# Kernel tuning notes

Hardware: AMD Instinct MI355X
Metric: run time of the kernel (lower is better)

The kernel has to match this reference:

```python
import jax, jax.numpy as jnp
import numpy as np
from jax import lax


def _haar_filters():
    c = np.float32(1.0 / np.sqrt(2.0))
    lo = np.array([c, c], np.float32)   # db1 dec_lo reversed == rec_lo == [c, c]
    hi = np.array([c, -c], np.float32)  # db1 dec_hi reversed == rec_hi == [c, -c]
    # filters[k][i, j] built exactly as in the torch source (outer products)
    dec = np.stack([np.outer(lo, lo) / 2.0, np.outer(hi, lo), np.outer(lo, hi), np.outer(hi, hi)]).astype(np.float32)
    inv = np.stack([np.outer(lo, lo) * 2.0, np.outer(hi, lo), np.outer(lo, hi), np.outer(hi, hi)]).astype(np.float32)
    return jnp.asarray(dec), jnp.asarray(inv)

DEC, INV = _haar_filters()  # each [4, 2, 2]


def wt(x):
    # depthwise Haar DWT, stride-2 2x2 conv per channel, then (v+1)/2 on high bands
    B, C, H, W = x.shape
    xr = x.reshape(B, C, H // 2, 2, W // 2, 2)
    out = jnp.einsum('bchiwj,kij->bckhw', xr, DEC)  # [B, C, 4, H/2, W/2]
    out = jnp.concatenate([out[:, :, :1], (out[:, :, 1:] + 1.0) * 0.5], axis=2)
    return out.reshape(B, 4 * C, H // 2, W // 2)


def iwt(v):
    # undo affine (2v-1 on high bands), then depthwise 2x2-stride-2 transpose conv
    B, C4, H, W = v.shape
    C = C4 // 4
    vr = v.reshape(B, C, 4, H, W)
    vr = jnp.concatenate([vr[:, :, :1], 2.0 * vr[:, :, 1:] - 1.0], axis=2)
    out = jnp.einsum('bckhw,kij->bchiwj', vr, INV)  # place each pixel into a 2x2 block
    return out.reshape(B, C, 2 * H, 2 * W)


def conv3x3(x, w, b):
    y = lax.conv_general_dilated(x, w, (1, 1), ((1, 1), (1, 1)),
                                 dimension_numbers=('NCHW', 'OIHW', 'NCHW'))
    return y + b[None, :, None, None]


def lrelu(x):
    return jnp.where(x >= 0, x, 0.2 * x)


def setup_inputs() -> dict:
    key = jax.random.key(0)
    ks = jax.random.split(key, 32)
    c = 16
    s = 0.02
    def w(k, shp):
        return jax.random.normal(ks[k], shp, jnp.float32) * s
    inp = {
        'x': jax.random.normal(ks[0], (4, 3, 256, 256), jnp.float32),
        'conv1_w': w(1, (c, 12, 3, 3)),        'conv1_b': w(2, (c,)),
        'conv2_w': w(3, (4 * c, 4 * c, 3, 3)), 'conv2_b': w(4, (4 * c,)),
        'conv3_w': w(5, (16 * c, 16 * c, 3, 3)), 'conv3_b': w(6, (16 * c,)),
        'conv4_w': w(7, (64 * c, 64 * c, 3, 3)), 'conv4_b': w(8, (64 * c,)),
        'convd4_w': w(9, (16 * c, 32 * c, 3, 3)), 'convd4_b': w(10, (16 * c,)),
        'convd3_w': w(11, (4 * c, 8 * c, 3, 3)), 'convd3_b': w(12, (4 * c,)),
        'convd2_w': w(13, (c, 2 * c, 3, 3)),    'convd2_b': w(14, (c,)),
        'convd1_w': w(15, (12, c, 3, 3)),       'convd1_b': w(16, (12,)),
        'cfin_w': w(17, (3, 3, 1, 1)),
    }
    return inp


def reference(x, conv1_w, conv1_b, conv2_w, conv2_b, conv3_w, conv3_b,
              conv4_w, conv4_b, convd4_w, convd4_b, convd3_w, convd3_b,
              convd2_w, convd2_b, convd1_w, convd1_b, cfin_w):
    w1 = wt(x)
    c1 = lrelu(conv3x3(w1, conv1_w, conv1_b))
    w2 = wt(c1)
    c2 = lrelu(conv3x3(w2, conv2_w, conv2_b))
    w3 = wt(c2)
    c3 = lrelu(conv3x3(w3, conv3_w, conv3_b))
    w4 = wt(c3)
    c4 = lrelu(conv3x3(w4, conv4_w, conv4_b))
    c5 = lrelu(conv3x3(c4, conv4_w, conv4_b))
    c6 = conv3x3(c5, conv4_w, conv4_b)
    ic4 = lrelu(c6 + w4)
    iw4 = jnp.concatenate([c3, iwt(ic4)], axis=1)
    ic3 = lrelu(conv3x3(iw4, convd4_w, convd4_b))
    iw3 = jnp.concatenate([c2, iwt(ic3)], axis=1)
    ic2 = lrelu(conv3x3(iw3, convd3_w, convd3_b))
    iw2 = jnp.concatenate([c1, iwt(ic2)], axis=1)
    ic1 = lrelu(conv3x3(iw2, convd2_w, convd2_b))
    iw1 = lrelu(conv3x3(ic1, convd1_w, convd1_b))
    y = iwt(iw1)
    # final 1x1 conv, no bias
    return jnp.einsum('bchw,oc->bohw', y, cfin_w[:, :, 0, 0])
```

## Files before the change

### kernel.cpp

```cpp
#include <hip/hip_runtime.h>


#define TPB 256

typedef _Float16 f16x8 __attribute__((ext_vector_type(8)));
typedef float f32x4 __attribute__((ext_vector_type(4)));

#define GLOAD_LDS16(g, l)                                                     \
    __builtin_amdgcn_global_load_lds(                                         \
        (const __attribute__((address_space(1))) void*)(g),                   \
        (__attribute__((address_space(3))) void*)(l), 16, 0, 0)

__global__ __launch_bounds__(TPB) void wt_k(const float* __restrict__ src,
                                            float* __restrict__ dst,
                                            int C, int H2, int W2) {
    int n = C * H2 * W2;
    int idx = blockIdx.x * TPB + threadIdx.x;
    if (idx >= n) return;
    int b = blockIdx.z;
    int c = idx / (H2 * W2);
    int p = idx - c * (H2 * W2);
    int h = p / W2, w = p - h * W2;
    int W = 2 * W2;
    const float* r = src + (((size_t)b * C + c) * (2 * H2) + 2 * h) * W + 2 * w;
    float a = r[0], bb = r[1], cc = r[W], dd = r[W + 1];
    size_t st = (size_t)H2 * W2;
    float* o = dst + (((size_t)b * 4 * C + 4 * c) * st) + p;
    o[0]      = 0.25f * (a + bb + cc + dd);
    o[st]     = (0.5f * (a + bb - cc - dd) + 1.0f) * 0.5f;
    o[2 * st] = (0.5f * (a - bb + cc - dd) + 1.0f) * 0.5f;
    o[3 * st] = (0.5f * (a - bb - cc + dd) + 1.0f) * 0.5f;
}

template <int LC>
__global__ __launch_bounds__(TPB) void wt_cl_k(const float* __restrict__ src,
                                               _Float16* __restrict__ X,
                                               int H2, int W2) {
    const int C = 1 << LC;
    int idx = blockIdx.x * TPB + threadIdx.x;
    int b = blockIdx.z;
    int c = idx & (C - 1);
    int p = idx >> LC;
    if (p >= H2 * W2) return;
    int h = p / W2, w = p - h * W2;
    int W = 2 * W2;
    const float* r = src + (((size_t)b * C + c) * (2 * H2) + 2 * h) * W + 2 * w;
    float a = r[0], bb = r[1], cc = r[W], dd = r[W + 1];
    _Float16* o = X + ((size_t)(b * H2 * W2 + p)) * (4 * C) + 4 * c;
    o[0] = (_Float16)(0.25f * (a + bb + cc + dd));
    o[1] = (_Float16)((0.5f * (a + bb - cc - dd) + 1.0f) * 0.5f);
    o[2] = (_Float16)((0.5f * (a - bb + cc - dd) + 1.0f) * 0.5f);
    o[3] = (_Float16)((0.5f * (a - bb - cc + dd) + 1.0f) * 0.5f);
}

__global__ __launch_bounds__(TPB) void iwt_k(const float* __restrict__ src,
                                             float* __restrict__ dst,
                                             int C, int H, int W) {
    int n = C * H * W;
    int idx = blockIdx.x * TPB + threadIdx.x;
    if (idx >= n) return;
    int b = blockIdx.z;
    int c = idx / (H * W);
    int p = idx - c * (H * W);
    int h = p / W, w = p - h * W;
    size_t st = (size_t)H * W;
    const float* r = src + ((size_t)b * 4 * C + 4 * c) * st + p;
    float v0 = r[0];
    float v1 = 2.0f * r[st] - 1.0f;
    float v2 = 2.0f * r[2 * st] - 1.0f;
    float v3 = 2.0f * r[3 * st] - 1.0f;
    float* o = dst + (((size_t)b * C + c) * (2 * H) + 2 * h) * (2 * W) + 2 * w;
    o[0]         = v0 + 0.5f * ( v1 + v2 + v3);
    o[1]         = v0 + 0.5f * ( v1 - v2 - v3);
    o[2 * W]     = v0 + 0.5f * (-v1 + v2 - v3);
    o[2 * W + 1] = v0 + 0.5f * (-v1 - v2 + v3);
}

template <int LC>
__global__ __launch_bounds__(TPB) void iwt_cl_k(const float* __restrict__ src,
                                                _Float16* __restrict__ X,
                                                int H, int W, int Coff, int Ctot) {
    const int C = 1 << LC;
    int idx = blockIdx.x * TPB + threadIdx.x;
    int b = blockIdx.z;
    int c = idx & (C - 1);
    int p = idx >> LC;
    if (p >= H * W) return;
    int h = p / W, w = p - h * W;
    size_t st = (size_t)H * W;
    const float* r = src + ((size_t)b * 4 * C + 4 * c) * st + p;
    float v0 = r[0];
    float v1 = 2.0f * r[st] - 1.0f;
    float v2 = 2.0f * r[2 * st] - 1.0f;
    float v3 = 2.0f * r[3 * st] - 1.0f;
    size_t mb = (size_t)b * 4 * H * W + (size_t)(2 * h) * (2 * W) + 2 * w;
    _Float16* o = X + mb * Ctot + Coff + c;
    o[0]                          = (_Float16)(v0 + 0.5f * ( v1 + v2 + v3));
    o[(size_t)Ctot]               = (_Float16)(v0 + 0.5f * ( v1 - v2 - v3));
    o[(size_t)(2 * W) * Ctot]     = (_Float16)(v0 + 0.5f * (-v1 + v2 - v3));
    o[(size_t)(2 * W + 1) * Ctot] = (_Float16)(v0 + 0.5f * (-v1 - v2 + v3));
}

template <int CO, bool LRELU, bool HAS_SKIP>
__global__ __launch_bounds__(TPB) void conv3x3_k(
    const float* __restrict__ s0, int C0,
    const float* __restrict__ s1,
    const float* __restrict__ wgt, const float* __restrict__ bias,
    const float* __restrict__ skip,
    float* __restrict__ out,
    int Cin, int Cout, int H, int W) {
    const int hw = H * W;
    int p = blockIdx.x * TPB + threadIdx.x;
    if (p >= hw) return;
    const int b = blockIdx.z;
    const int cog = blockIdx.y * CO;
    const int h = p / W, w = p - (p / W) * W;
    const bool hm = h > 0, hp = h < H - 1, wm = w > 0, wpp = w < W - 1;

    float acc[CO];
#pragma unroll
    for (int i = 0; i < CO; i++) acc[i] = bias[cog + i];

    const int C1n = Cin - C0;
    for (int ci = 0; ci < Cin; ci++) {
        const float* sp = (ci < C0)
            ? s0 + ((size_t)b * C0 + ci) * hw
            : s1 + ((size_t)b * C1n + (ci - C0)) * hw;
        const float* r = sp + p;
        float x00 = (hm && wm)  ? r[-W - 1] : 0.0f;
        float x01 = hm          ? r[-W]     : 0.0f;
        float x02 = (hm && wpp) ? r[-W + 1] : 0.0f;
        float x10 = wm          ? r[-1]     : 0.0f;
        float x11 =               r[0];
        float x12 = wpp         ? r[1]      : 0.0f;
        float x20 = (hp && wm)  ? r[W - 1]  : 0.0f;
        float x21 = hp          ? r[W]      : 0.0f;
        float x22 = (hp && wpp) ? r[W + 1]  : 0.0f;
        const float* wk = wgt + ((size_t)cog * Cin + ci) * 9;
#pragma unroll
        for (int i = 0; i < CO; i++) {
            const float* wi = wk + (size_t)i * Cin * 9;
            acc[i] += x00 * wi[0] + x01 * wi[1] + x02 * wi[2]
                    + x10 * wi[3] + x11 * wi[4] + x12 * wi[5]
                    + x20 * wi[6] + x21 * wi[7] + x22 * wi[8];
        }
    }
#pragma unroll
    for (int i = 0; i < CO; i++) {
        float v = acc[i];
        if (HAS_SKIP) v += skip[((size_t)b * Cout + cog + i) * hw + p];
        if (LRELU) v = (v >= 0.0f) ? v : 0.2f * v;
        out[((size_t)b * Cout + cog + i) * hw + p] = v;
    }
}


__global__ __launch_bounds__(TPB) void wtrans_g_k(const float* __restrict__ w,
                                                  _Float16* __restrict__ Bh,
                                                  int Cin, int n) {
    int idx = blockIdx.x * TPB + threadIdx.x;
    if (idx >= n) return;
    int K = 9 * Cin;
    int co = idx / K;
    int r = idx - co * K;
    int tap = r / Cin, ci = r - tap * Cin;
    Bh[idx] = (_Float16)w[((size_t)co * Cin + ci) * 9 + tap];
}

__global__ __launch_bounds__(TPB) void bias_mc_k(float* __restrict__ C,
                                                 const float* __restrict__ bias,
                                                 int mask) {
    int idx = blockIdx.x * TPB + threadIdx.x;
    C[idx] = bias[idx & mask];
}

__global__ __launch_bounds__(TPB) void w4_to_x_k(const float* __restrict__ W4,
                                                 _Float16* __restrict__ X) {
    int idx = blockIdx.x * TPB + threadIdx.x;
    int m = idx >> 10, ci = idx & 1023;
    int b = m >> 8, p = m & 255;
    X[idx] = (_Float16)W4[(((size_t)b << 10) + ci) * 256 + p];
}

template <int LC, int NT>
__global__ __launch_bounds__(TPB) void cgemm_k(
    const _Float16* __restrict__ X,
    const _Float16* __restrict__ Bw,
    float* __restrict__ Cout,
    int Wimg, int kc, int N) {
    constexpr int CIN = 1 << LC;
    constexpr int K = 9 << LC;
    const int HW = Wimg * Wimg;
    const int m0 = blockIdx.x * 128;
    const int n0 = blockIdx.y * (NT * 32);
    const int k0 = blockIdx.z * kc;
    const int iters = kc >> 5;

    __shared__ _Float16 As[128 * 32];
    __shared__ _Float16 Bs[NT * 32 * 32];

    const int tid = threadIdx.x;
    const int wave = tid >> 6, lane = tid & 63;
    const int wm = (wave >> 1) * 64;
    const int wn = (wave & 1) * (NT * 16);

    const int r0 = tid >> 2;
    const int colh = (tid & 3) * 8;
    int rbase[2], rh[2], rw[2];
#pragma unroll
    for (int q = 0; q < 2; q++) {
        int m = m0 + r0 + q * 64;
        int b = m / HW;
        int p = m - b * HW;
        rh[q] = p / Wimg;
        rw[q] = p - rh[q] * Wimg;
        rbase[q] = b * HW;
    }
    _Float16* lA0 = &As[r0 * 32 + colh];
    _Float16* lA1 = &As[(r0 + 64) * 32 + colh];

    const int f = tid * 16;
    const int brow = f >> 6, bbyte = f & 63;
    const char* gB[NT / 2];
#pragma unroll
    for (int q = 0; q < NT / 2; q++)
        gB[q] = (const char*)Bw + ((size_t)(n0 + brow + q * 64) * K + k0) * 2 + bbyte;

    f32x4 acc[4][NT];
#pragma unroll
    for (int i = 0; i < 4; i++)
#pragma unroll
        for (int j = 0; j < NT; j++) acc[i][j] = {0.f, 0.f, 0.f, 0.f};

    const int frow = lane & 15;
    const int fkh = (lane >> 4) * 8;

    for (int it = 0; it < iters; ++it) {
        const int kk = k0 + (it << 5);
        const int tap = kk >> LC;
        const int ci0 = kk & (CIN - 1);
        const int t3 = tap / 3;
        const int dh = t3 - 1;
        const int dw = tap - t3 * 3 - 1;
#pragma unroll
        for (int q = 0; q < 2; q++) {
            int hh = rh[q] + dh, ww = rw[q] + dw;
            f16x8 v = {0, 0, 0, 0, 0, 0, 0, 0};
            if ((unsigned)hh < (unsigned)Wimg && (unsigned)ww < (unsigned)Wimg)
                v = *(const f16x8*)(X + (((size_t)(rbase[q] + hh * Wimg + ww)) << LC)
                                      + ci0 + colh);
            if (q == 0) *(f16x8*)lA0 = v;
            else        *(f16x8*)lA1 = v;
        }
#pragma unroll
        for (int q = 0; q < NT / 2; q++) {
            GLOAD_LDS16(gB[q], (char*)Bs + f + q * 4096);
            gB[q] += 64;
        }
        __syncthreads();

        f16x8 af[4], bf[NT];
#pragma unroll
        for (int mt = 0; mt < 4; mt++)
            af[mt] = *(const f16x8*)&As[(wm + mt * 16 + frow) * 32 + fkh];
#pragma unroll
        for (int nt = 0; nt < NT; nt++)
            bf[nt] = *(const f16x8*)&Bs[(wn + nt * 16 + frow) * 32 + fkh];
#pragma unroll
        for (int mt = 0; mt < 4; mt++)
#pragma unroll
            for (int nt = 0; nt < NT; nt++)
                acc[mt][nt] = __builtin_amdgcn_mfma_f32_16x16x32_f16(
                    af[mt], bf[nt], acc[mt][nt], 0, 0, 0);
        __syncthreads();
    }

    const int cm = m0 + wm + (lane >> 4) * 4;
    const int cn = n0 + wn + (lane & 15);
#pragma unroll
    for (int mt = 0; mt < 4; mt++)
#pragma unroll
        for (int nt = 0; nt < NT; nt++)
#pragma unroll
            for (int r = 0; r < 4; r++)
                unsafeAtomicAdd(&Cout[(size_t)(cm + mt * 16 + r) * N + cn + nt * 16],
                                acc[mt][nt][r]);
}

template <bool SPAT, bool CL>
__global__ __launch_bounds__(TPB) void fin_cl_k(const float* __restrict__ Cm,
                                                float* __restrict__ spat,
                                                _Float16* __restrict__ X,
                                                int LN, int LHW, int Coff, int Ctot) {
    int idx = blockIdx.x * TPB + threadIdx.x;
    int m = idx >> LN;
    int c = idx & ((1 << LN) - 1);
    float v = Cm[idx];
    v = (v >= 0.0f) ? v : 0.2f * v;
    if (SPAT) {
        int b = m >> LHW;
        int p = m & ((1 << LHW) - 1);
        spat[(((size_t)(b << LN) + c) << LHW) + p] = v;
    }
    if (CL) X[(size_t)m * Ctot + Coff + c] = (_Float16)v;
}

__global__ __launch_bounds__(TPB) void fin_sp_k(const float* __restrict__ C,
                                                const float* __restrict__ W4,
                                                float* __restrict__ out) {
    int idx = blockIdx.x * TPB + threadIdx.x;
    int b = idx >> 18;
    int r = idx & 262143;
    int c = r >> 8, p = r & 255;
    int m = (b << 8) + p;
    float v = C[(size_t)m * 1024 + c] + W4[idx];
    out[idx] = (v >= 0.0f) ? v : 0.2f * v;
}

__global__ __launch_bounds__(TPB) void final_k(const float* __restrict__ src,
                                               const float* __restrict__ cf,
                                               float* __restrict__ out) {
    int p = blockIdx.x * TPB + threadIdx.x;
    int b = blockIdx.z;
    int h = p >> 7, w = p & 127;
    const int st = 128 * 128;
    float y00[3], y01[3], y10[3], y11[3];
    const float* r = src + (size_t)b * 12 * st + p;
#pragma unroll
    for (int c = 0; c < 3; c++) {
        float v0 = r[(4 * c) * st];
        float v1 = 2.0f * r[(4 * c + 1) * st] - 1.0f;
        float v2 = 2.0f * r[(4 * c + 2) * st] - 1.0f;
        float v3 = 2.0f * r[(4 * c + 3) * st] - 1.0f;
        y00[c] = v0 + 0.5f * ( v1 + v2 + v3);
        y01[c] = v0 + 0.5f * ( v1 - v2 - v3);
        y10[c] = v0 + 0.5f * (-v1 + v2 - v3);
        y11[c] = v0 + 0.5f * (-v1 - v2 + v3);
    }
#pragma unroll
    for (int o = 0; o < 3; o++) {
        float k0 = cf[o * 3], k1 = cf[o * 3 + 1], k2 = cf[o * 3 + 2];
        float* q = out + (((size_t)b * 3 + o) * 256 + 2 * h) * 256 + 2 * w;
        q[0]   = k0 * y00[0] + k1 * y00[1] + k2 * y00[2];
        q[1]   = k0 * y01[0] + k1 * y01[1] + k2 * y01[2];
        q[256] = k0 * y10[0] + k1 * y10[1] + k2 * y10[2];
        q[257] = k0 * y11[0] + k1 * y11[1] + k2 * y11[2];
    }
}

static inline void conv_launch(const float* s0, int C0, const float* s1,
                               const float* wgt, const float* bias,
                               float* out, int Cin, int Cout, int H, int W,
                               int CO, hipStream_t st) {
    dim3 grid((H * W + TPB - 1) / TPB, Cout / CO, 4);
    if (CO == 8)
        conv3x3_k<8, true, false><<<grid, TPB, 0, st>>>(s0, C0, s1, wgt, bias, nullptr, out, Cin, Cout, H, W);
    else
        conv3x3_k<4, true, false><<<grid, TPB, 0, st>>>(s0, C0, s1, wgt, bias, nullptr, out, Cin, Cout, H, W);
}

extern "C" void kernel_launch(void* const* d_in, const int* in_sizes, int n_in,
                              void* d_out, int out_size, void* d_ws, size_t ws_size,
                              hipStream_t stream) {
    (void)in_sizes; (void)n_in; (void)out_size; (void)ws_size;
    const float* x      = (const float*)d_in[0];
    const float* c1w    = (const float*)d_in[1];
    const float* c1b    = (const float*)d_in[2];
    const float* c2w    = (const float*)d_in[3];
    const float* c2b    = (const float*)d_in[4];
    const float* c3w    = (const float*)d_in[5];
    const float* c3b    = (const float*)d_in[6];
    const float* c4w    = (const float*)d_in[7];
    const float* c4b    = (const float*)d_in[8];
    const float* d4w    = (const float*)d_in[9];
    const float* d4b    = (const float*)d_in[10];
    const float* d3w    = (const float*)d_in[11];
    const float* d3b    = (const float*)d_in[12];
    const float* d2w    = (const float*)d_in[13];
    const float* d2b    = (const float*)d_in[14];
    const float* d1w    = (const float*)d_in[15];
    const float* d1b    = (const float*)d_in[16];
    const float* cfin   = (const float*)d_in[17];
    float* out = (float*)d_out;

    char* base = (char*)d_ws;
    const size_t MB = 1 << 20;
    float*    C1   = (float*)(base + 0 * MB);
    float*    C3   = (float*)(base + 4 * MB);
    float*    W4   = (float*)(base + 8 * MB);
    float*    TA   = (float*)(base + 12 * MB);
    float*    TB   = (float*)(base + 16 * MB);
    float*    C2   = (float*)(base + 20 * MB);
    float*    Cmc  = (float*)(base + 24 * MB);
    _Float16* X0   = (_Float16*)(base + 28 * MB);
    _Float16* X1   = (_Float16*)(base + 30 * MB);
    _Float16* Xa   = (_Float16*)(base + 32 * MB);
    _Float16* Xd3  = (_Float16*)(base + 34 * MB);
    _Float16* Xd4  = (_Float16*)(base + 38 * MB);
    _Float16* Bh4  = (_Float16*)(base + 42 * MB);
    _Float16* Bh3  = (_Float16*)(base + 60 * MB);
    _Float16* Bhd4 = (_Float16*)(base + 62 * MB);
    _Float16* Bhd3 = (_Float16*)(base + 65 * MB);
    _Float16* Bh2  = (_Float16*)(base + 66 * MB);

    wtrans_g_k<<<36864, TPB, 0, stream>>>(c4w, Bh4, 1024, 9437184);
    wtrans_g_k<<<2304,  TPB, 0, stream>>>(c3w, Bh3, 256, 589824);
    wtrans_g_k<<<4608,  TPB, 0, stream>>>(d4w, Bhd4, 512, 1179648);
    wtrans_g_k<<<288,   TPB, 0, stream>>>(d3w, Bhd3, 128, 73728);
    wtrans_g_k<<<144,   TPB, 0, stream>>>(c2w, Bh2, 64, 36864);

    wt_k<<<dim3(192, 1, 4), TPB, 0, stream>>>(x, TA, 3, 128, 128);
    conv_launch(TA, 12, nullptr, c1w, c1b, C1, 12, 16, 128, 128, 8, stream);
    wt_cl_k<4><<<dim3(256, 1, 4), TPB, 0, stream>>>(C1, Xa, 64, 64);
    bias_mc_k<<<4096, TPB, 0, stream>>>(Cmc, c2b, 63);
    cgemm_k<6, 2><<<dim3(128, 1, 2), TPB, 0, stream>>>(Xa, Bh2, Cmc, 64, 288, 64);
    fin_cl_k<true, true><<<4096, TPB, 0, stream>>>(Cmc, C2, Xd3, 6, 12, 0, 128);
    wt_cl_k<6><<<dim3(256, 1, 4), TPB, 0, stream>>>(C2, Xa, 32, 32);
    bias_mc_k<<<4096, TPB, 0, stream>>>(Cmc, c3b, 255);
    cgemm_k<8, 4><<<dim3(32, 2, 4), TPB, 0, stream>>>(Xa, Bh3, Cmc, 32, 576, 256);
    fin_cl_k<true, true><<<4096, TPB, 0, stream>>>(Cmc, C3, Xd4, 8, 10, 0, 512);
    wt_k<<<dim3(256, 1, 4), TPB, 0, stream>>>(C3, W4, 256, 16, 16);
    w4_to_x_k<<<4096, TPB, 0, stream>>>(W4, X0);
    bias_mc_k<<<4096, TPB, 0, stream>>>(Cmc, c4b, 1023);
    cgemm_k<10, 4><<<dim3(8, 8, 8), TPB, 0, stream>>>(X0, Bh4, Cmc, 16, 1152, 1024);
    fin_cl_k<false, true><<<4096, TPB, 0, stream>>>(Cmc, nullptr, X1, 10, 8, 0, 1024);
    bias_mc_k<<<4096, TPB, 0, stream>>>(Cmc, c4b, 1023);
    cgemm_k<10, 4><<<dim3(8, 8, 8), TPB, 0, stream>>>(X1, Bh4, Cmc, 16, 1152, 1024);
    fin_cl_k<false, true><<<4096, TPB, 0, stream>>>(Cmc, nullptr, X0, 10, 8, 0, 1024);
    bias_mc_k<<<4096, TPB, 0, stream>>>(Cmc, c4b, 1023);
    cgemm_k<10, 4><<<dim3(8, 8, 8), TPB, 0, stream>>>(X0, Bh4, Cmc, 16, 1152, 1024);
    fin_sp_k<<<4096, TPB, 0, stream>>>(Cmc, W4, TA);
    iwt_cl_k<8><<<dim3(256, 1, 4), TPB, 0, stream>>>(TA, Xd4, 16, 16, 256, 512);
    bias_mc_k<<<4096, TPB, 0, stream>>>(Cmc, d4b, 255);
    cgemm_k<9, 4><<<dim3(32, 2, 4), TPB, 0, stream>>>(Xd4, Bhd4, Cmc, 32, 1152, 256);
    fin_cl_k<true, false><<<4096, TPB, 0, stream>>>(Cmc, TA, nullptr, 8, 10, 0, 0);
    iwt_cl_k<6><<<dim3(256, 1, 4), TPB, 0, stream>>>(TA, Xd3, 32, 32, 64, 128);
    bias_mc_k<<<4096, TPB, 0, stream>>>(Cmc, d3b, 63);
    cgemm_k<7, 2><<<dim3(128, 1, 2), TPB, 0, stream>>>(Xd3, Bhd3, Cmc, 64, 576, 64);
    fin_cl_k<true, false><<<4096, TPB, 0, stream>>>(Cmc, TA, nullptr, 6, 12, 0, 0);
    iwt_k<<<dim3(256, 1, 4), TPB, 0, stream>>>(TA, TB, 16, 64, 64);
    conv_launch(C1, 16, TB, d2w, d2b, TA, 32, 16, 128, 128, 8, stream);
    conv_launch(TA, 16, TA, d1w, d1b, TB, 16, 12, 128, 128, 4, stream);
    final_k<<<dim3(64, 1, 4), TPB, 0, stream>>>(TB, cfin, out);
}
```

Measured before the change: 638.7 us.

## Double-buffer conv GEMM, pre-swizzle weights, fuse bias init and dual-layout DWT

The implicit-GEMM conv kernel now double-buffers its A and B LDS tiles, prefetching the next k-slice while MFMAs run on the current one. Weights are pre-swizzled into fragment order so B staging is one contiguous load per thread and fragment reads are conflict-free. Bias initialisation of the next accumulator is folded into the previous finalize kernel, and a combined DWT writes both the spatial and channel-last fp16 copies, removing several small launches. Split-K factors are raised for the smaller GEMMs to add parallelism, at the cost of more atomic adds.

```diff
diff --git a/kernel.cpp b/kernel.cpp
--- a/kernel.cpp
+++ b/kernel.cpp
@@ -30,6 +30,27 @@
     o[st]     = (0.5f * (a + bb - cc - dd) + 1.0f) * 0.5f;
     o[2 * st] = (0.5f * (a - bb + cc - dd) + 1.0f) * 0.5f;
     o[3 * st] = (0.5f * (a - bb - cc + dd) + 1.0f) * 0.5f;
+}
+
+__global__ __launch_bounds__(TPB) void wt_dual_k(const float* __restrict__ src,
+                                                 float* __restrict__ dst,
+                                                 _Float16* __restrict__ X) {
+    int idx = blockIdx.x * TPB + threadIdx.x;
+    int b = blockIdx.z;
+    int c = idx >> 8;
+    int p = idx & 255;
+    int h = p >> 4, w = p & 15;
+    const float* r = src + (((size_t)b * 256 + c) * 32 + 2 * h) * 32 + 2 * w;
+    float a = r[0], bb = r[1], cc = r[32], dd = r[33];
+    float v0 = 0.25f * (a + bb + cc + dd);
+    float v1 = (0.5f * (a + bb - cc - dd) + 1.0f) * 0.5f;
+    float v2 = (0.5f * (a - bb + cc - dd) + 1.0f) * 0.5f;
+    float v3 = (0.5f * (a - bb - cc + dd) + 1.0f) * 0.5f;
+    float* o = dst + (((size_t)b * 1024 + 4 * c) * 256) + p;
+    o[0] = v0; o[256] = v1; o[512] = v2; o[768] = v3;
+    _Float16* q = X + ((size_t)(b * 256 + p)) * 1024 + 4 * c;
+    q[0] = (_Float16)v0; q[1] = (_Float16)v1;
+    q[2] = (_Float16)v2; q[3] = (_Float16)v3;
 }
 
 template <int LC>
@@ -155,15 +176,21 @@
 }
 
 
-__global__ __launch_bounds__(TPB) void wtrans_g_k(const float* __restrict__ w,
-                                                  _Float16* __restrict__ Bh,
-                                                  int Cin, int n) {
+__global__ __launch_bounds__(TPB) void wtrans_sw_k(const float* __restrict__ w,
+                                                   _Float16* __restrict__ Bh,
+                                                   int Cin, int KB, int n) {
     int idx = blockIdx.x * TPB + threadIdx.x;
     if (idx >= n) return;
-    int K = 9 * Cin;
-    int co = idx / K;
-    int r = idx - co * K;
-    int tap = r / Cin, ci = r - tap * Cin;
+    int e = idx & 7;
+    int lane = (idx >> 3) & 63;
+    int sub = (idx >> 9) & 3;
+    int chunk = idx >> 11;
+    int kb = chunk % KB;
+    int nb = chunk / KB;
+    int co = nb * 64 + sub * 16 + (lane & 15);
+    int k = kb * 32 + ((lane >> 4) & 3) * 8 + e;
+    int tap = k / Cin;
+    int ci = k - tap * Cin;
     Bh[idx] = (_Float16)w[((size_t)co * Cin + ci) * 9 + tap];
 }
 
@@ -172,14 +199,6 @@
                                                  int mask) {
     int idx = blockIdx.x * TPB + threadIdx.x;
     C[idx] = bias[idx & mask];
-}
-
-__global__ __launch_bounds__(TPB) void w4_to_x_k(const float* __restrict__ W4,
-                                                 _Float16* __restrict__ X) {
-    int idx = blockIdx.x * TPB + threadIdx.x;
-    int m = idx >> 10, ci = idx & 1023;
-    int b = m >> 8, p = m & 255;
-    X[idx] = (_Float16)W4[(((size_t)b << 10) + ci) * 256 + p];
 }
 
 template <int LC, int NT>
@@ -189,42 +208,71 @@
     float* __restrict__ Cout,
     int Wimg, int kc, int N) {
     constexpr int CIN = 1 << LC;
-    constexpr int K = 9 << LC;
+    constexpr int Kd = 9 << LC;
+    constexpr int KB = Kd >> 5;
     const int HW = Wimg * Wimg;
     const int m0 = blockIdx.x * 128;
     const int n0 = blockIdx.y * (NT * 32);
     const int k0 = blockIdx.z * kc;
     const int iters = kc >> 5;
 
-    __shared__ _Float16 As[128 * 32];
-    __shared__ _Float16 Bs[NT * 32 * 32];
+    __shared__ _Float16 As[2][4096];
+    __shared__ _Float16 Bs[2][NT * 1024];
 
     const int tid = threadIdx.x;
     const int wave = tid >> 6, lane = tid & 63;
     const int wm = (wave >> 1) * 64;
     const int wn = (wave & 1) * (NT * 16);
 
-    const int r0 = tid >> 2;
-    const int colh = (tid & 3) * 8;
-    int rbase[2], rh[2], rw[2];
+    int rh[2], rw[2], rbase[2], cq[2];
 #pragma unroll
     for (int q = 0; q < 2; q++) {
-        int m = m0 + r0 + q * 64;
+        int a16 = tid + q * 256;
+        int t = a16 >> 6, l = a16 & 63;
+        int row = t * 16 + (l & 15);
+        cq[q] = ((l >> 4) & 3) * 8;
+        int m = m0 + row;
         int b = m / HW;
         int p = m - b * HW;
         rh[q] = p / Wimg;
         rw[q] = p - rh[q] * Wimg;
         rbase[q] = b * HW;
     }
-    _Float16* lA0 = &As[r0 * 32 + colh];
-    _Float16* lA1 = &As[(r0 + 64) * 32 + colh];
-
-    const int f = tid * 16;
-    const int brow = f >> 6, bbyte = f & 63;
-    const char* gB[NT / 2];
-#pragma unroll
-    for (int q = 0; q < NT / 2; q++)
-        gB[q] = (const char*)Bw + ((size_t)(n0 + brow + q * 64) * K + k0) * 2 + bbyte;
+
+    const int nb0 = n0 >> 6;
+    const int kb0 = k0 >> 5;
+
+#define STAGE_B(it, dbuf)                                                       \
+    {                                                                           \
+        int kb = kb0 + (it);                                                    \
+        const char* g0 = (const char*)Bw +                                      \
+            ((size_t)(nb0 * KB + kb) * 2048 + (size_t)tid * 8) * 2;             \
+        GLOAD_LDS16(g0, (char*)&Bs[dbuf][0] + tid * 16);                        \
+        if (NT == 4) {                                                          \
+            const char* g1 = (const char*)Bw +                                  \
+                ((size_t)((nb0 + 1) * KB + kb) * 2048 + (size_t)tid * 8) * 2;   \
+            GLOAD_LDS16(g1, (char*)&Bs[dbuf][2048] + tid * 16);                 \
+        }                                                                       \
+    }
+
+#define LOAD_A(it, a0v, a1v)                                                    \
+    {                                                                           \
+        const int kk = k0 + ((it) << 5);                                        \
+        const int tap = kk >> LC;                                               \
+        const int ci0 = kk & (CIN - 1);                                         \
+        const int t3 = tap / 3;                                                 \
+        const int dh = t3 - 1, dwv = tap - t3 * 3 - 1;                          \
+        int hh0 = rh[0] + dh, ww0 = rw[0] + dwv;                                \
+        a0v = (f16x8){0, 0, 0, 0, 0, 0, 0, 0};                                  \
+        if ((unsigned)hh0 < (unsigned)Wimg && (unsigned)ww0 < (unsigned)Wimg)   \
+            a0v = *(const f16x8*)(X +                                           \
+                (((size_t)(rbase[0] + hh0 * Wimg + ww0)) << LC) + ci0 + cq[0]); \
+        int hh1 = rh[1] + dh, ww1 = rw[1] + dwv;                                \
+        a1v = (f16x8){0, 0, 0, 0, 0, 0, 0, 0};                                  \
+        if ((unsigned)hh1 < (unsigned)Wimg && (unsigned)ww1 < (unsigned)Wimg)   \
+            a1v = *(const f16x8*)(X +                                           \
+                (((size_t)(rbase[1] + hh1 * Wimg + ww1)) << LC) + ci0 + cq[1]); \
+    }
 
     f32x4 acc[4][NT];
 #pragma unroll
@@ -232,48 +280,42 @@
 #pragma unroll
         for (int j = 0; j < NT; j++) acc[i][j] = {0.f, 0.f, 0.f, 0.f};
 
-    const int frow = lane & 15;
-    const int fkh = (lane >> 4) * 8;
-
+    f16x8 a0, a1;
+    STAGE_B(0, 0);
+    LOAD_A(0, a0, a1);
+    *(f16x8*)&As[0][(size_t)tid * 8] = a0;
+    *(f16x8*)&As[0][(size_t)(tid + 256) * 8] = a1;
+    __syncthreads();
+
+    int buf = 0;
     for (int it = 0; it < iters; ++it) {
-        const int kk = k0 + (it << 5);
-        const int tap = kk >> LC;
-        const int ci0 = kk & (CIN - 1);
-        const int t3 = tap / 3;
-        const int dh = t3 - 1;
-        const int dw = tap - t3 * 3 - 1;
-#pragma unroll
-        for (int q = 0; q < 2; q++) {
-            int hh = rh[q] + dh, ww = rw[q] + dw;
-            f16x8 v = {0, 0, 0, 0, 0, 0, 0, 0};
-            if ((unsigned)hh < (unsigned)Wimg && (unsigned)ww < (unsigned)Wimg)
-                v = *(const f16x8*)(X + (((size_t)(rbase[q] + hh * Wimg + ww)) << LC)
-                                      + ci0 + colh);
-            if (q == 0) *(f16x8*)lA0 = v;
-            else        *(f16x8*)lA1 = v;
+        const bool more = (it + 1) < iters;
+        if (more) {
+            STAGE_B(it + 1, buf ^ 1);
+            LOAD_A(it + 1, a0, a1);
         }
-#pragma unroll
-        for (int q = 0; q < NT / 2; q++) {
-            GLOAD_LDS16(gB[q], (char*)Bs + f + q * 4096);
-            gB[q] += 64;
-        }
-        __syncthreads();
-
         f16x8 af[4], bf[NT];
 #pragma unroll
         for (int mt = 0; mt < 4; mt++)
-            af[mt] = *(const f16x8*)&As[(wm + mt * 16 + frow) * 32 + fkh];
+            af[mt] = *(const f16x8*)&As[buf][((wm >> 4) + mt) * 512 + lane * 8];
 #pragma unroll
         for (int nt = 0; nt < NT; nt++)
-            bf[nt] = *(const f16x8*)&Bs[(wn + nt * 16 + frow) * 32 + fkh];
+            bf[nt] = *(const f16x8*)&Bs[buf][((wn >> 4) + nt) * 512 + lane * 8];
 #pragma unroll
         for (int mt = 0; mt < 4; mt++)
 #pragma unroll
             for (int nt = 0; nt < NT; nt++)
                 acc[mt][nt] = __builtin_amdgcn_mfma_f32_16x16x32_f16(
                     af[mt], bf[nt], acc[mt][nt], 0, 0, 0);
+        if (more) {
+            *(f16x8*)&As[buf ^ 1][(size_t)tid * 8] = a0;
+            *(f16x8*)&As[buf ^ 1][(size_t)(tid + 256) * 8] = a1;
+        }
         __syncthreads();
-    }
+        buf ^= 1;
+    }
+#undef STAGE_B
+#undef LOAD_A
 
     const int cm = m0 + wm + (lane >> 4) * 4;
     const int cn = n0 + wn + (lane & 15);
@@ -287,11 +329,13 @@
                                 acc[mt][nt][r]);
 }
 
-template <bool SPAT, bool CL>
-__global__ __launch_bounds__(TPB) void fin_cl_k(const float* __restrict__ Cm,
+template <bool SPAT, bool CL, bool NB>
+__global__ __launch_bounds__(TPB) void fin_cl_k(float* __restrict__ Cm,
                                                 float* __restrict__ spat,
                                                 _Float16* __restrict__ X,
-                                                int LN, int LHW, int Coff, int Ctot) {
+                                                int LN, int LHW, int Coff, int Ctot,
+                                                const float* __restrict__ nbias,
+                                                int nmask) {
     int idx = blockIdx.x * TPB + threadIdx.x;
     int m = idx >> LN;
     int c = idx & ((1 << LN) - 1);
@@ -303,18 +347,24 @@
         spat[(((size_t)(b << LN) + c) << LHW) + p] = v;
     }
     if (CL) X[(size_t)m * Ctot + Coff + c] = (_Float16)v;
-}
-
-__global__ __launch_bounds__(TPB) void fin_sp_k(const float* __restrict__ C,
+    if (NB) Cm[idx] = nbias[idx & nmask];
+}
+
+template <bool NB>
+__global__ __launch_bounds__(TPB) void fin_sp_k(float* __restrict__ Cm,
                                                 const float* __restrict__ W4,
-                                                float* __restrict__ out) {
+                                                float* __restrict__ out,
+                                                const float* __restrict__ nbias,
+                                                int nmask) {
     int idx = blockIdx.x * TPB + threadIdx.x;
     int b = idx >> 18;
     int r = idx & 262143;
     int c = r >> 8, p = r & 255;
     int m = (b << 8) + p;
-    float v = C[(size_t)m * 1024 + c] + W4[idx];
+    size_t pos = (size_t)m * 1024 + c;
+    float v = Cm[pos] + W4[idx];
     out[idx] = (v >= 0.0f) ? v : 0.2f * v;
+    if (NB) Cm[pos] = nbias[((int)pos) & nmask];
 }
 
 __global__ __launch_bounds__(TPB) void final_k(const float* __restrict__ src,
@@ -403,41 +453,34 @@
     _Float16* Bhd3 = (_Float16*)(base + 65 * MB);
     _Float16* Bh2  = (_Float16*)(base + 66 * MB);
 
-    wtrans_g_k<<<36864, TPB, 0, stream>>>(c4w, Bh4, 1024, 9437184);
-    wtrans_g_k<<<2304,  TPB, 0, stream>>>(c3w, Bh3, 256, 589824);
-    wtrans_g_k<<<4608,  TPB, 0, stream>>>(d4w, Bhd4, 512, 1179648);
-    wtrans_g_k<<<288,   TPB, 0, stream>>>(d3w, Bhd3, 128, 73728);
-    wtrans_g_k<<<144,   TPB, 0, stream>>>(c2w, Bh2, 64, 36864);
+    wtrans_sw_k<<<36864, TPB, 0, stream>>>(c4w, Bh4, 1024, 288, 9437184);
+    wtrans_sw_k<<<2304,  TPB, 0, stream>>>(c3w, Bh3, 256, 72, 589824);
+    wtrans_sw_k<<<4608,  TPB, 0, stream>>>(d4w, Bhd4, 512, 144, 1179648);
+    wtrans_sw_k<<<288,   TPB, 0, stream>>>(d3w, Bhd3, 128, 36, 73728);
+    wtrans_sw_k<<<144,   TPB, 0, stream>>>(c2w, Bh2, 64, 18, 36864);
 
     wt_k<<<dim3(192, 1, 4), TPB, 0, stream>>>(x, TA, 3, 128, 128);
     conv_launch(TA, 12, nullptr, c1w, c1b, C1, 12, 16, 128, 128, 8, stream);
     wt_cl_k<4><<<dim3(256, 1, 4), TPB, 0, stream>>>(C1, Xa, 64, 64);
     bias_mc_k<<<4096, TPB, 0, stream>>>(Cmc, c2b, 63);
-    cgemm_k<6, 2><<<dim3(128, 1, 2), TPB, 0, stream>>>(Xa, Bh2, Cmc, 64, 288, 64);
-    fin_cl_k<true, true><<<4096, TPB, 0, stream>>>(Cmc, C2, Xd3, 6, 12, 0, 128);
+    cgemm_k<6, 2><<<dim3(128, 1, 3), TPB, 0, stream>>>(Xa, Bh2, Cmc, 64, 192, 64);
+    fin_cl_k<true, true, true><<<4096, TPB, 0, stream>>>(Cmc, C2, Xd3, 6, 12, 0, 128, c3b, 255);
     wt_cl_k<6><<<dim3(256, 1, 4), TPB, 0, stream>>>(C2, Xa, 32, 32);
-    bias_mc_k<<<4096, TPB, 0, stream>>>(Cmc, c3b, 255);
-    cgemm_k<8, 4><<<dim3(32, 2, 4), TPB, 0, stream>>>(Xa, Bh3, Cmc, 32, 576, 256);
-    fin_cl_k<true, true><<<4096, TPB, 0, stream>>>(Cmc, C3, Xd4, 8, 10, 0, 512);
-    wt_k<<<dim3(256, 1, 4), TPB, 0, stream>>>(C3, W4, 256, 16, 16);
-    w4_to_x_k<<<4096, TPB, 0, stream>>>(W4, X0);
-    bias_mc_k<<<4096, TPB, 0, stream>>>(Cmc, c4b, 1023);
+    cgemm_k<8, 4><<<dim3(32, 2, 8), TPB, 0, stream>>>(Xa, Bh3, Cmc, 32, 288, 256);
+    fin_cl_k<true, true, true><<<4096, TPB, 0, stream>>>(Cmc, C3, Xd4, 8, 10, 0, 512, c4b, 1023);
+    wt_dual_k<<<dim3(256, 1, 4), TPB, 0, stream>>>(C3, W4, X0);
     cgemm_k<10, 4><<<dim3(8, 8, 8), TPB, 0, stream>>>(X0, Bh4, Cmc, 16, 1152, 1024);
-    fin_cl_k<false, true><<<4096, TPB, 0, stream>>>(Cmc, nullptr, X1, 10, 8, 0, 1024);
-    bias_mc_k<<<4096, TPB, 0, stream>>>(Cmc, c4b, 1023);
+    fin_cl_k<false, true, true><<<4096, TPB, 0, stream>>>(Cmc, nullptr, X1, 10, 8, 0, 1024, c4b, 1023);
     cgemm_k<10, 4><<<dim3(8, 8, 8), TPB, 0, stream>>>(X1, Bh4, Cmc, 16, 1152, 1024);
-    fin_cl_k<false, true><<<4096, TPB, 0, stream>>>(Cmc, nullptr, X0, 10, 8, 0, 1024);
-    bias_mc_k<<<4096, TPB, 0, stream>>>(Cmc, c4b, 1023);
+    fin_cl_k<false, true, true><<<4096, TPB, 0, stream>>>(Cmc, nullptr, X0, 10, 8, 0, 1024, c4b, 1023);
     cgemm_k<10, 4><<<dim3(8, 8, 8), TPB, 0, stream>>>(X0, Bh4, Cmc, 16, 1152, 1024);
-    fin_sp_k<<<4096, TPB, 0, stream>>>(Cmc, W4, TA);
+    fin_sp_k<true><<<4096, TPB, 0, stream>>>(Cmc, W4, TA, d4b, 255);
     iwt_cl_k<8><<<dim3(256, 1, 4), TPB, 0, stream>>>(TA, Xd4, 16, 16, 256, 512);
-    bias_mc_k<<<4096, TPB, 0, stream>>>(Cmc, d4b, 255);
-    cgemm_k<9, 4><<<dim3(32, 2, 4), TPB, 0, stream>>>(Xd4, Bhd4, Cmc, 32, 1152, 256);
-    fin_cl_k<true, false><<<4096, TPB, 0, stream>>>(Cmc, TA, nullptr, 8, 10, 0, 0);
+    cgemm_k<9, 4><<<dim3(32, 2, 8), TPB, 0, stream>>>(Xd4, Bhd4, Cmc, 32, 576, 256);
+    fin_cl_k<true, false, true><<<4096, TPB, 0, stream>>>(Cmc, TA, nullptr, 8, 10, 0, 0, d3b, 63);
     iwt_cl_k<6><<<dim3(256, 1, 4), TPB, 0, stream>>>(TA, Xd3, 32, 32, 64, 128);
-    bias_mc_k<<<4096, TPB, 0, stream>>>(Cmc, d3b, 63);
-    cgemm_k<7, 2><<<dim3(128, 1, 2), TPB, 0, stream>>>(Xd3, Bhd3, Cmc, 64, 576, 64);
-    fin_cl_k<true, false><<<4096, TPB, 0, stream>>>(Cmc, TA, nullptr, 6, 12, 0, 0);
+    cgemm_k<7, 2><<<dim3(128, 1, 4), TPB, 0, stream>>>(Xd3, Bhd3, Cmc, 64, 288, 64);
+    fin_cl_k<true, false, false><<<4096, TPB, 0, stream>>>(Cmc, TA, nullptr, 6, 12, 0, 0, nullptr, 0);
     iwt_k<<<dim3(256, 1, 4), TPB, 0, stream>>>(TA, TB, 16, 64, 64);
     conv_launch(C1, 16, TB, d2w, d2b, TA, 32, 16, 128, 128, 8, stream);
     conv_launch(TA, 16, TA, d1w, d1b, TB, 16, 12, 128, 128, 4, stream);
```

New measurement: 608.9 us. 4.7% less time.
